# Kernel tuning notes

Hardware: AMD Instinct MI355X
Metric: run time of the kernel (lower is better)

Reference implementation:

```python
import jax, jax.numpy as jnp
import numpy as np

D_MODEL, D_HIDDEN, N_EXPERTS = 1024, 4096, 8
CAP_FACTOR, LBL_COEF, ZLOSS_COEF = 1.25, 0.01, 0.0


def setup_inputs() -> dict:
    key = jax.random.key(0)
    ks = jax.random.split(key, 4)
    B, T = 4, 2048
    x = jax.random.normal(ks[0], (B, T, D_MODEL), dtype=jnp.float32)
    # router linear
    Wr = jax.random.normal(ks[1], (D_MODEL, N_EXPERTS), jnp.float32) / np.sqrt(D_MODEL).astype(np.float32)
    br = jnp.zeros((N_EXPERTS,), jnp.float32)
    # per-expert MLP: fc1 [D->H], gelu, fc2 [H->D]
    W1 = jax.random.normal(ks[2], (N_EXPERTS, D_MODEL, D_HIDDEN), jnp.float32) / np.sqrt(D_MODEL).astype(np.float32)
    b1 = jnp.zeros((N_EXPERTS, D_HIDDEN), jnp.float32)
    W2 = jax.random.normal(ks[3], (N_EXPERTS, D_HIDDEN, D_MODEL), jnp.float32) / np.sqrt(D_HIDDEN).astype(np.float32)
    b2 = jnp.zeros((N_EXPERTS, D_MODEL), jnp.float32)
    return {"x": x, "Wr": Wr, "br": br, "W1": W1, "b1": b1, "W2": W2, "b2": b2}


def reference(x, Wr, br, W1, b1, W2, b2):
    B, T, D = x.shape
    N = B * T
    E = Wr.shape[1]
    cap = int(CAP_FACTOR * (N / E) + 1)  # static Python int

    h = x.reshape(N, D)
    # --- Top1Router ---
    logits = h @ Wr + br                              # [N, E]
    probs = jax.nn.softmax(logits, axis=-1)
    top1 = jnp.argmax(probs, axis=-1)                 # [N]
    w = jnp.take_along_axis(probs, top1[:, None], axis=1)  # [N, 1]
    assign = jax.nn.one_hot(top1, E, dtype=jnp.float32)    # constant wrt grads
    importance = probs.mean(axis=0)
    load = jax.lax.stop_gradient(assign).mean(axis=0)
    lb_loss = E * jnp.sum(importance * load)
    z_loss = jnp.mean(jax.nn.logsumexp(logits, axis=-1) ** 2)

    # --- capacity-based dispatch (first `cap` tokens per expert, token order) ---
    pos = (jnp.cumsum(assign, axis=0) * assign).sum(axis=-1).astype(jnp.int32) - 1  # [N] slot within expert
    keep = pos < cap
    slot = jnp.where(keep, pos, cap)  # dropped tokens -> overflow slot `cap`
    xe = jnp.zeros((E, cap + 1, D), x.dtype).at[top1, slot].set(h)[:, :cap]  # [E, cap, D]

    # --- per-expert MLP as grouped GEMMs ---
    he = jax.nn.gelu(jnp.einsum('ecd,edh->ech', xe, W1) + b1[:, None, :])    # [E, cap, H]
    ye = jnp.einsum('ech,ehd->ecd', he, W2) + b2[:, None, :]                 # [E, cap, D]

    # --- combine (gather back, scale by router weight, zero dropped) ---
    out = ye[top1, jnp.minimum(pos, cap - 1)] * w   # [N, D]
    out = jnp.where(keep[:, None], out, jnp.zeros((), x.dtype))
    y = out.reshape(B, T, D)
    aux = LBL_COEF * lb_loss + ZLOSS_COEF * z_loss
    return (y, aux)
```

## Files before the change

### kernel.cpp

```cpp
#include <hip/hip_runtime.h>
#include <hip/hip_bf16.h>

#define N_TOK 8192
#define DM    1024
#define DH    4096
#define NE    8
#define CAP   1281
#define CAPR  1408
#define ISTR  1536

typedef unsigned short u16;
typedef __attribute__((ext_vector_type(8))) __bf16 bf16x8;
typedef __attribute__((ext_vector_type(8))) short short8;
typedef __attribute__((ext_vector_type(4))) short s16x4;
typedef __attribute__((ext_vector_type(4))) float f4;

__device__ __forceinline__ u16 f2bf(float f){
  union { float f; unsigned u; } v; v.f = f;
  unsigned r = v.u + 0x7fffu + ((v.u >> 16) & 1u);
  return (u16)(r >> 16);
}

__device__ __forceinline__ float gelu_fast(float v){
  float u = 0.7978845608028654f * (v + 0.044715f * v * v * v);
  return v * __builtin_amdgcn_rcpf(1.0f + __expf(-2.0f * u));
}

__device__ __forceinline__ void gl2lds16(const void* g, void* l){
  __builtin_amdgcn_global_load_lds((const __attribute__((address_space(1))) void*)g,
                                   (__attribute__((address_space(3))) void*)l, 16, 0, 0);
}

__global__ __launch_bounds__(256) void tcvt_k(const float* __restrict__ in, u16* __restrict__ out,
                                              int K, int Nn){
  __shared__ float tile[64][68];
  size_t mb = (size_t)blockIdx.z * (size_t)K * (size_t)Nn;
  const float* ip = in + mb;
  u16* op = out + mb;
  int n0 = blockIdx.x*64, k0 = blockIdx.y*64;
  int t = threadIdx.x;
  int kr = t>>4, nc = (t&15)*4;
  #pragma unroll
  for (int ii=0;ii<4;ii++){
    f4 v = *(const f4*)&ip[(size_t)(k0+kr+16*ii)*Nn + n0 + nc];
    tile[kr+16*ii][nc+0] = v[0]; tile[kr+16*ii][nc+1] = v[1];
    tile[kr+16*ii][nc+2] = v[2]; tile[kr+16*ii][nc+3] = v[3];
  }
  __syncthreads();
  int nr = t>>2, kc = (t&3)*16;
  short8 o0, o1;
  #pragma unroll
  for (int c=0;c<8;c++){
    o0[c] = (short)f2bf(tile[kc+c][nr]);
    o1[c] = (short)f2bf(tile[kc+8+c][nr]);
  }
  *(short8*)&op[(size_t)(n0+nr)*K + k0 + kc] = o0;
  *(short8*)&op[(size_t)(n0+nr)*K + k0 + kc + 8] = o1;
}

__global__ __launch_bounds__(256) void router_k(const float* __restrict__ x, const float* __restrict__ Wr,
    const float* __restrict__ br, u16* __restrict__ Xb, int* __restrict__ top1,
    float* __restrict__ wgt, float* __restrict__ impSum){
  __shared__ float pSh[4][8];
  int wid = threadIdx.x >> 6, lane = threadIdx.x & 63;
  int n = blockIdx.x * 4 + wid;
  const float* xr = x + (size_t)n * DM;
  u16* xbr = Xb + (size_t)n * DM;
  float acc[8];
  #pragma unroll
  for (int e=0;e<8;e++) acc[e]=0.f;
  #pragma unroll
  for (int c=0;c<4;c++){
    int d0 = c*256 + lane*4;
    f4 xv = *(const f4*)(xr + d0);
    s16x4 xb;
    #pragma unroll
    for (int j=0;j<4;j++) xb[j] = (short)f2bf(xv[j]);
    *(s16x4*)(xbr + d0) = xb;
    #pragma unroll
    for (int j=0;j<4;j++){
      const float* wrow = Wr + (size_t)(d0+j)*NE;
      float xs = xv[j];
      #pragma unroll
      for (int e=0;e<8;e++) acc[e] = fmaf(xs, wrow[e], acc[e]);
    }
  }
  #pragma unroll
  for (int off=32; off>0; off>>=1){
    #pragma unroll
    for (int e=0;e<8;e++) acc[e] += __shfl_down(acc[e], off, 64);
  }
  if (lane==0){
    float lg[8]; float mx = -1e30f;
    #pragma unroll
    for (int e=0;e<8;e++){ lg[e] = acc[e] + br[e]; mx = fmaxf(mx, lg[e]); }
    float p[8], s=0.f;
    #pragma unroll
    for (int e=0;e<8;e++){ p[e] = expf(lg[e]-mx); s += p[e]; }
    int bt=0; float bv=lg[0];
    #pragma unroll
    for (int e=1;e<8;e++){ if (lg[e]>bv){ bv=lg[e]; bt=e; } }
    float inv = 1.f/s;
    top1[n] = bt; wgt[n] = p[bt]*inv;
    #pragma unroll
    for (int e=0;e<8;e++) pSh[wid][e] = p[e]*inv;
  }
  __syncthreads();
  if (threadIdx.x < 8){
    int e = threadIdx.x;
    atomicAdd(&impSum[e], pSh[0][e]+pSh[1][e]+pSh[2][e]+pSh[3][e]);
  }
}

__global__ __launch_bounds__(1024) void scan_k(const int* __restrict__ top1, int* __restrict__ idx,
    int* __restrict__ cnt, int* __restrict__ rawcnt, int* __restrict__ dropList,
    int* __restrict__ nDrop, const float* __restrict__ impSum, float* __restrict__ auxOut){
  __shared__ int waveCnt[16][8];
  __shared__ int wavePre[16][8];
  __shared__ int chunkTot[8];
  __shared__ int base_s[8];
  int tid = threadIdx.x, wid = tid>>6, lane = tid&63;
  if (tid < 8) base_s[tid] = 0;
  __syncthreads();
  for (int c=0;c<8;c++){
    int t = c*1024 + tid;
    int e = top1[t];
    int myPre = 0;
    #pragma unroll
    for (int ex=0; ex<8; ex++){
      unsigned long long mk = __ballot(e == ex);
      if (lane == 0) waveCnt[wid][ex] = __popcll(mk);
      if (ex == e) myPre = __popcll(mk & ((1ull<<lane)-1ull));
    }
    __syncthreads();
    if (tid < 8){
      int run = 0;
      for (int wv=0; wv<16; wv++){ wavePre[wv][tid] = run; run += waveCnt[wv][tid]; }
      chunkTot[tid] = run;
    }
    __syncthreads();
    int pos = base_s[e] + wavePre[wid][e] + myPre;
    if (pos < CAP) idx[e*ISTR + pos] = t;
    else { int d = atomicAdd(nDrop, 1); dropList[d] = t; }
    __syncthreads();
    if (tid < 8) base_s[tid] += chunkTot[tid];
    __syncthreads();
  }
  if (tid < 8){
    rawcnt[tid] = base_s[tid];
    cnt[tid] = base_s[tid] < CAP ? base_s[tid] : CAP;
  }
  if (tid == 0){
    float s = 0.f;
    for (int e=0;e<8;e++) s += (impSum[e]*(1.f/N_TOK)) * ((float)base_s[e]*(1.f/N_TOK));
    *auxOut = 0.01f * 8.f * s;
  }
}

__global__ __launch_bounds__(256) void zdrop_k(const int* __restrict__ dropList,
    const int* __restrict__ nDrop, float* __restrict__ y){
  int nd = *nDrop;
  for (int i = blockIdx.x; i < nd; i += gridDim.x){
    int t = dropList[i];
    f4* row = (f4*)(y + (size_t)t * DM);
    f4 z; z[0]=0.f; z[1]=0.f; z[2]=0.f; z[3]=0.f;
    row[threadIdx.x] = z;
  }
}


#define LDA(buf, m, kk) (*(const bf16x8*)&lds[(buf)*16384 + (aBase ^ ((kk)*32)) + (m)*1024])
#define LDB(buf, n, kk) (*(const bf16x8*)&lds[32768 + (buf)*16384 + (bBase ^ ((kk)*32)) + (n)*1024])

#define SA_J(buf, j, kc) gl2lds16(aS[j] + (size_t)(kc)*64, &lds[(buf)*16384 + ((j)*512 + t)*8])
#define SB_ALLM(buf, kc) do{ \
  gl2lds16(bS[0] + (size_t)(kc)*64, &lds[32768 + (buf)*16384 + (0*512 + t)*8]); \
  gl2lds16(bS[1] + (size_t)(kc)*64, &lds[32768 + (buf)*16384 + (1*512 + t)*8]); \
  gl2lds16(bS[2] + (size_t)(kc)*64, &lds[32768 + (buf)*16384 + (2*512 + t)*8]); \
  gl2lds16(bS[3] + (size_t)(kc)*64, &lds[32768 + (buf)*16384 + (3*512 + t)*8]); }while(0)

#define LGKM0 do{ asm volatile("s_waitcnt lgkmcnt(0)" ::: "memory"); \
                  __builtin_amdgcn_sched_barrier(0); }while(0)

#define MFMA_PAIR(q) \
  _Pragma("unroll") for (int j_=0;j_<2;j_++) \
    _Pragma("unroll") for (int n_=0;n_<4;n_++) \
      _Pragma("unroll") for (int kk_=0;kk_<2;kk_++) \
        acc[2*(q)+j_][n_] = __builtin_amdgcn_mfma_f32_16x16x32_bf16(a_[j_][kk_], Bf[n_][kk_], acc[2*(q)+j_][n_], 0,0,0);

#define KTILE(buf, ktv, NTv) do{ \
  int kc1 = (ktv)+1 < (NTv) ? (ktv)+1 : (NTv)-1; \
  int kc2 = (ktv)+2 < (NTv) ? (ktv)+2 : (NTv)-1; \
  bf16x8 a_[2][2]; \
   \
  asm volatile("s_waitcnt vmcnt(6)" ::: "memory"); \
  __builtin_amdgcn_s_barrier(); \
  _Pragma("unroll") for (int n_=0;n_<4;n_++){ Bf[n_][0] = LDB(buf,n_,0); Bf[n_][1] = LDB(buf,n_,1); } \
  a_[0][0]=LDA(buf,0,0); a_[0][1]=LDA(buf,0,1); a_[1][0]=LDA(buf,1,0); a_[1][1]=LDA(buf,1,1); \
  SA_J((buf)^1, 1, kc1); SA_J((buf)^1, 3, kc1); \
  LGKM0; \
  __builtin_amdgcn_s_setprio(1); MFMA_PAIR(0); __builtin_amdgcn_s_setprio(0); \
   \
  __builtin_amdgcn_s_barrier(); \
  a_[0][0]=LDA(buf,2,0); a_[0][1]=LDA(buf,2,1); a_[1][0]=LDA(buf,3,0); a_[1][1]=LDA(buf,3,1); \
  SB_ALLM(buf, kc2); \
  LGKM0; \
  __builtin_amdgcn_s_setprio(1); MFMA_PAIR(1); __builtin_amdgcn_s_setprio(0); \
   \
  __builtin_amdgcn_s_barrier(); \
  a_[0][0]=LDA(buf,4,0); a_[0][1]=LDA(buf,4,1); a_[1][0]=LDA(buf,5,0); a_[1][1]=LDA(buf,5,1); \
  SA_J(buf, 0, kc2); SA_J(buf, 2, kc2); \
  LGKM0; \
  __builtin_amdgcn_s_setprio(1); MFMA_PAIR(2); __builtin_amdgcn_s_setprio(0); \
   \
  __builtin_amdgcn_s_barrier(); \
  a_[0][0]=LDA(buf,6,0); a_[0][1]=LDA(buf,6,1); a_[1][0]=LDA(buf,7,0); a_[1][1]=LDA(buf,7,1); \
  LGKM0; \
  __builtin_amdgcn_s_setprio(1); MFMA_PAIR(3); __builtin_amdgcn_s_setprio(0); \
}while(0)

#define GEMM_PROLOGUE() do{ \
  SB_ALLM(0, 0); \
  SA_J(0,0,0); SA_J(0,2,0); \
  SA_J(0,1,0); SA_J(0,3,0); \
  SB_ALLM(1, 1); \
  SA_J(1,0,1); SA_J(1,2,1); }while(0)

__global__ __launch_bounds__(512, 2) void gemm1_k(
    const u16* __restrict__ Xb, const u16* __restrict__ W1T,
    const float* __restrict__ b1, const int* __restrict__ idx,
    const int* __restrict__ cnt, u16* __restrict__ He)
{
  int e = blockIdx.z, mt = blockIdx.y, nt = blockIdx.x;
  int cn = cnt[e];
  if (mt*256 >= cn) return;
  __shared__ __align__(16) u16 lds[65536];
  int t = threadIdx.x, lane = t&63, wid = t>>6;
  int waveM = wid>>2, waveN = wid&3;
  int rA = lane&15, kb = lane>>4, s = rA&7;

  const u16* aS[4]; const u16* bS[4];
  #pragma unroll
  for (int j=0;j<4;j++){
    int pos = j*512 + t;
    int row = pos>>3, ch = pos&7;
    int gcb = ch ^ (row&7);
    int slotrow = mt*256 + row;
    int token = (slotrow < cn) ? idx[e*ISTR + slotrow] : 0;
    aS[j] = Xb + (size_t)token*DM + gcb*8;
    bS[j] = W1T + ((size_t)e*DH + nt*256 + row)*DM + gcb*8;
  }
  f4 acc[8][4];
  #pragma unroll
  for (int m=0;m<8;m++)
    #pragma unroll
    for (int n=0;n<4;n++)
      #pragma unroll
      for (int j=0;j<4;j++) acc[m][n][j]=0.f;

  int aBase = (waveM*128 + rA)*64 + (kb ^ s)*8;
  int bBase = (waveN*64  + rA)*64 + (kb ^ s)*8;
  bf16x8 Bf[4][2];

  GEMM_PROLOGUE();
  const int NT = DM/64;
  #pragma unroll 1
  for (int i=0;i<NT/2;i++){
    KTILE(0, 2*i,   NT);
    KTILE(1, 2*i+1, NT);
  }
  asm volatile("s_waitcnt vmcnt(0) lgkmcnt(0)" ::: "memory");

  int rG = lane>>4;
  #pragma unroll
  for (int n=0;n<4;n++){
    int col = nt*256 + waveN*64 + n*16 + rA;
    float bias = b1[e*DH + col];
    #pragma unroll
    for (int m=0;m<8;m++){
      int slot = mt*256 + waveM*128 + m*16 + rG*4;
      if (slot < CAPR){
        u16* dst = He + ((size_t)e*CAPR + slot)*DH + col;
        #pragma unroll
        for (int j=0;j<4;j++){
          float v = acc[m][n][j] + bias;
          dst[(size_t)j*DH] = f2bf(gelu_fast(v));
        }
      }
    }
  }
}

__global__ __launch_bounds__(512, 2) void gemm2_k(
    const u16* __restrict__ He, const u16* __restrict__ W2T,
    const float* __restrict__ b2, const int* __restrict__ idx,
    const int* __restrict__ cnt, const float* __restrict__ wgt,
    float* __restrict__ y)
{
  int e = blockIdx.z, mt = blockIdx.y, nt = blockIdx.x;
  int cn = cnt[e];
  if (mt*256 >= cn) return;
  __shared__ __align__(16) u16 lds[65536];
  int t = threadIdx.x, lane = t&63, wid = t>>6;
  int waveM = wid>>2, waveN = wid&3;
  int rA = lane&15, kb = lane>>4, s = rA&7;

  const u16* aS[4]; const u16* bS[4];
  #pragma unroll
  for (int j=0;j<4;j++){
    int pos = j*512 + t;
    int row = pos>>3, ch = pos&7;
    int gcb = ch ^ (row&7);
    int srow = mt*256 + row; if (srow >= cn) srow = cn-1;
    aS[j] = He  + ((size_t)e*CAPR + srow)*DH + gcb*8;
    bS[j] = W2T + ((size_t)e*DM + nt*256 + row)*DH + gcb*8;
  }
  f4 acc[8][4];
  #pragma unroll
  for (int m=0;m<8;m++)
    #pragma unroll
    for (int n=0;n<4;n++)
      #pragma unroll
      for (int j=0;j<4;j++) acc[m][n][j]=0.f;

  int aBase = (waveM*128 + rA)*64 + (kb ^ s)*8;
  int bBase = (waveN*64  + rA)*64 + (kb ^ s)*8;
  bf16x8 Bf[4][2];

  GEMM_PROLOGUE();
  const int NT = DH/64;
  #pragma unroll 1
  for (int i=0;i<NT/2;i++){
    KTILE(0, 2*i,   NT);
    KTILE(1, 2*i+1, NT);
  }
  asm volatile("s_waitcnt vmcnt(0) lgkmcnt(0)" ::: "memory");

  int rG = lane>>4;
  float bias_[4];
  #pragma unroll
  for (int n=0;n<4;n++) bias_[n] = b2[e*DM + nt*256 + waveN*64 + n*16 + rA];
  #pragma unroll
  for (int m=0;m<8;m++){
    int slot0 = mt*256 + waveM*128 + m*16 + rG*4;
    #pragma unroll
    for (int j=0;j<4;j++){
      int slot = slot0 + j;
      bool valid = slot < cn;
      int tk = valid ? idx[e*ISTR + slot] : 0;
      float wv = valid ? wgt[tk] : 0.f;
      float* yr = y + (size_t)tk*DM;
      #pragma unroll
      for (int n=0;n<4;n++){
        int col = nt*256 + waveN*64 + n*16 + rA;
        if (valid) yr[col] = (acc[m][n][j] + bias_[n]) * wv;
      }
    }
  }
}

extern "C" void kernel_launch(void* const* d_in, const int* in_sizes, int n_in,
                              void* d_out, int out_size, void* d_ws, size_t ws_size,
                              hipStream_t stream){
  const float* x  = (const float*)d_in[0];
  const float* Wr = (const float*)d_in[1];
  const float* br = (const float*)d_in[2];
  const float* W1 = (const float*)d_in[3];
  const float* b1 = (const float*)d_in[4];
  const float* W2 = (const float*)d_in[5];
  const float* b2 = (const float*)d_in[6];
  float* y = (float*)d_out;

  char* ws = (char*)d_ws;
  u16* Xb  = (u16*)(ws);
  u16* W1T = (u16*)(ws + 16777216ull);
  u16* W2T = (u16*)(ws + 16777216ull + 67108864ull);
  u16* He  = (u16*)(ws + 16777216ull + 2ull*67108864ull);
  char* tail = ws + 16777216ull + 2ull*67108864ull + (size_t)NE*CAPR*DH*2ull;
  int*   top1 = (int*)(tail);
  float* wgt  = (float*)(tail + 32768);
  int*   idx  = (int*)(tail + 65536);
  int*   drop = (int*)(tail + 65536 + 49152);
  float* impSum = (float*)(tail + 65536 + 49152 + 32768);
  int*   nDrop  = (int*)((char*)impSum + 32);
  int*   cnt    = nDrop + 1;
  int*   rawcnt = cnt + 8;

  (void)hipMemsetAsync(impSum, 0, 64, stream);

  tcvt_k<<<dim3(64,16,8), 256, 0, stream>>>(W1, W1T, DM, DH);
  tcvt_k<<<dim3(16,64,8), 256, 0, stream>>>(W2, W2T, DH, DM);
  router_k<<<2048, 256, 0, stream>>>(x, Wr, br, Xb, top1, wgt, impSum);
  scan_k<<<1, 1024, 0, stream>>>(top1, idx, cnt, rawcnt, drop, nDrop, impSum,
                                 y + (size_t)N_TOK*DM);
  zdrop_k<<<64, 256, 0, stream>>>(drop, nDrop, y);
  gemm1_k<<<dim3(DH/256, 6, NE), 512, 0, stream>>>(Xb, W1T, b1, idx, cnt, He);
  gemm2_k<<<dim3(DM/256, 6, NE), 512, 0, stream>>>(He, W2T, b2, idx, cnt, wgt, y);

  (void)in_sizes; (void)n_in; (void)out_size; (void)ws_size;
}
```

Measured before the change: 356.2 us.

## Replace pipelined 256x256 GEMM tiles with simple single-buffered 128x128 tiles

Both expert GEMMs drop the hand-scheduled double-buffered 256x256 pipeline (staggered global-to-LDS loads, setprio, partial waitcnts) for a plain 128x128 tile loop. Each k-step stages everything, syncs, computes and syncs again. The grid is retiled to 128-row and 128-column blocks with 256 threads. The unused rawcnt output is also removed. This gives smaller tiles and finer-grained blocks, but loses the overlap of loads with MFMA work and halves reuse per tile, so it is likely a simplification or debugging step rather than a speedup.

```diff
diff --git a/kernel.cpp b/kernel.cpp
--- a/kernel.cpp
+++ b/kernel.cpp
@@ -113,8 +113,8 @@
 }
 
 __global__ __launch_bounds__(1024) void scan_k(const int* __restrict__ top1, int* __restrict__ idx,
-    int* __restrict__ cnt, int* __restrict__ rawcnt, int* __restrict__ dropList,
-    int* __restrict__ nDrop, const float* __restrict__ impSum, float* __restrict__ auxOut){
+    int* __restrict__ cnt, int* __restrict__ dropList, int* __restrict__ nDrop,
+    const float* __restrict__ impSum, float* __restrict__ auxOut){
   __shared__ int waveCnt[16][8];
   __shared__ int wavePre[16][8];
   __shared__ int chunkTot[8];
@@ -147,7 +147,6 @@
     __syncthreads();
   }
   if (tid < 8){
-    rawcnt[tid] = base_s[tid];
     cnt[tid] = base_s[tid] < CAP ? base_s[tid] : CAP;
   }
   if (tid == 0){
@@ -169,129 +168,94 @@
 }
 
 
-#define LDA(buf, m, kk) (*(const bf16x8*)&lds[(buf)*16384 + (aBase ^ ((kk)*32)) + (m)*1024])
-#define LDB(buf, n, kk) (*(const bf16x8*)&lds[32768 + (buf)*16384 + (bBase ^ ((kk)*32)) + (n)*1024])
-
-#define SA_J(buf, j, kc) gl2lds16(aS[j] + (size_t)(kc)*64, &lds[(buf)*16384 + ((j)*512 + t)*8])
-#define SB_ALLM(buf, kc) do{ \
-  gl2lds16(bS[0] + (size_t)(kc)*64, &lds[32768 + (buf)*16384 + (0*512 + t)*8]); \
-  gl2lds16(bS[1] + (size_t)(kc)*64, &lds[32768 + (buf)*16384 + (1*512 + t)*8]); \
-  gl2lds16(bS[2] + (size_t)(kc)*64, &lds[32768 + (buf)*16384 + (2*512 + t)*8]); \
-  gl2lds16(bS[3] + (size_t)(kc)*64, &lds[32768 + (buf)*16384 + (3*512 + t)*8]); }while(0)
-
-#define LGKM0 do{ asm volatile("s_waitcnt lgkmcnt(0)" ::: "memory"); \
-                  __builtin_amdgcn_sched_barrier(0); }while(0)
-
-#define MFMA_PAIR(q) \
-  _Pragma("unroll") for (int j_=0;j_<2;j_++) \
-    _Pragma("unroll") for (int n_=0;n_<4;n_++) \
-      _Pragma("unroll") for (int kk_=0;kk_<2;kk_++) \
-        acc[2*(q)+j_][n_] = __builtin_amdgcn_mfma_f32_16x16x32_bf16(a_[j_][kk_], Bf[n_][kk_], acc[2*(q)+j_][n_], 0,0,0);
-
-#define KTILE(buf, ktv, NTv) do{ \
-  int kc1 = (ktv)+1 < (NTv) ? (ktv)+1 : (NTv)-1; \
-  int kc2 = (ktv)+2 < (NTv) ? (ktv)+2 : (NTv)-1; \
-  bf16x8 a_[2][2]; \
-   \
-  asm volatile("s_waitcnt vmcnt(6)" ::: "memory"); \
-  __builtin_amdgcn_s_barrier(); \
-  _Pragma("unroll") for (int n_=0;n_<4;n_++){ Bf[n_][0] = LDB(buf,n_,0); Bf[n_][1] = LDB(buf,n_,1); } \
-  a_[0][0]=LDA(buf,0,0); a_[0][1]=LDA(buf,0,1); a_[1][0]=LDA(buf,1,0); a_[1][1]=LDA(buf,1,1); \
-  SA_J((buf)^1, 1, kc1); SA_J((buf)^1, 3, kc1); \
-  LGKM0; \
-  __builtin_amdgcn_s_setprio(1); MFMA_PAIR(0); __builtin_amdgcn_s_setprio(0); \
-   \
-  __builtin_amdgcn_s_barrier(); \
-  a_[0][0]=LDA(buf,2,0); a_[0][1]=LDA(buf,2,1); a_[1][0]=LDA(buf,3,0); a_[1][1]=LDA(buf,3,1); \
-  SB_ALLM(buf, kc2); \
-  LGKM0; \
-  __builtin_amdgcn_s_setprio(1); MFMA_PAIR(1); __builtin_amdgcn_s_setprio(0); \
-   \
-  __builtin_amdgcn_s_barrier(); \
-  a_[0][0]=LDA(buf,4,0); a_[0][1]=LDA(buf,4,1); a_[1][0]=LDA(buf,5,0); a_[1][1]=LDA(buf,5,1); \
-  SA_J(buf, 0, kc2); SA_J(buf, 2, kc2); \
-  LGKM0; \
-  __builtin_amdgcn_s_setprio(1); MFMA_PAIR(2); __builtin_amdgcn_s_setprio(0); \
-   \
-  __builtin_amdgcn_s_barrier(); \
-  a_[0][0]=LDA(buf,6,0); a_[0][1]=LDA(buf,6,1); a_[1][0]=LDA(buf,7,0); a_[1][1]=LDA(buf,7,1); \
-  LGKM0; \
-  __builtin_amdgcn_s_setprio(1); MFMA_PAIR(3); __builtin_amdgcn_s_setprio(0); \
-}while(0)
-
-#define GEMM_PROLOGUE() do{ \
-  SB_ALLM(0, 0); \
-  SA_J(0,0,0); SA_J(0,2,0); \
-  SA_J(0,1,0); SA_J(0,3,0); \
-  SB_ALLM(1, 1); \
-  SA_J(1,0,1); SA_J(1,2,1); }while(0)
-
-__global__ __launch_bounds__(512, 2) void gemm1_k(
+#define LDA(m, kk) (*(const bf16x8*)&As[(aBase ^ ((kk)*32)) + (m)*1024])
+#define LDB(n, kk) (*(const bf16x8*)&Bs[(bBase ^ ((kk)*32)) + (n)*1024])
+
+#define STAGE_ALL(kc) do{ \
+  gl2lds16(aS[0] + (size_t)(kc)*64, &As[(0*256 + t)*8]); \
+  gl2lds16(aS[1] + (size_t)(kc)*64, &As[(1*256 + t)*8]); \
+  gl2lds16(aS[2] + (size_t)(kc)*64, &As[(2*256 + t)*8]); \
+  gl2lds16(aS[3] + (size_t)(kc)*64, &As[(3*256 + t)*8]); \
+  gl2lds16(bS[0] + (size_t)(kc)*64, &Bs[(0*256 + t)*8]); \
+  gl2lds16(bS[1] + (size_t)(kc)*64, &Bs[(1*256 + t)*8]); \
+  gl2lds16(bS[2] + (size_t)(kc)*64, &Bs[(2*256 + t)*8]); \
+  gl2lds16(bS[3] + (size_t)(kc)*64, &Bs[(3*256 + t)*8]); }while(0)
+
+#define COMPUTE_STEP() do{ \
+  _Pragma("unroll") \
+  for (int kk=0; kk<2; kk++){ \
+    bf16x8 af[4], bfr[4]; \
+    _Pragma("unroll") for (int m=0;m<4;m++) af[m] = LDA(m,kk); \
+    _Pragma("unroll") for (int n=0;n<4;n++) bfr[n] = LDB(n,kk); \
+    _Pragma("unroll") for (int m=0;m<4;m++) \
+      _Pragma("unroll") for (int n=0;n<4;n++) \
+        acc[m][n] = __builtin_amdgcn_mfma_f32_16x16x32_bf16(af[m], bfr[n], acc[m][n], 0,0,0); \
+  } }while(0)
+
+__global__ __launch_bounds__(256) void gemm1_k(
     const u16* __restrict__ Xb, const u16* __restrict__ W1T,
     const float* __restrict__ b1, const int* __restrict__ idx,
     const int* __restrict__ cnt, u16* __restrict__ He)
 {
   int e = blockIdx.z, mt = blockIdx.y, nt = blockIdx.x;
   int cn = cnt[e];
-  if (mt*256 >= cn) return;
-  __shared__ __align__(16) u16 lds[65536];
+  if (mt*128 >= cn) return;
+  __shared__ __align__(16) u16 As[128*64];
+  __shared__ __align__(16) u16 Bs[128*64];
   int t = threadIdx.x, lane = t&63, wid = t>>6;
-  int waveM = wid>>2, waveN = wid&3;
+  int waveM = wid>>1, waveN = wid&1;
   int rA = lane&15, kb = lane>>4, s = rA&7;
 
   const u16* aS[4]; const u16* bS[4];
   #pragma unroll
   for (int j=0;j<4;j++){
-    int pos = j*512 + t;
+    int pos = j*256 + t;
     int row = pos>>3, ch = pos&7;
     int gcb = ch ^ (row&7);
-    int slotrow = mt*256 + row;
+    int slotrow = mt*128 + row;
     int token = (slotrow < cn) ? idx[e*ISTR + slotrow] : 0;
     aS[j] = Xb + (size_t)token*DM + gcb*8;
-    bS[j] = W1T + ((size_t)e*DH + nt*256 + row)*DM + gcb*8;
-  }
-  f4 acc[8][4];
-  #pragma unroll
-  for (int m=0;m<8;m++)
+    bS[j] = W1T + ((size_t)e*DH + nt*128 + row)*DM + gcb*8;
+  }
+  f4 acc[4][4];
+  #pragma unroll
+  for (int m=0;m<4;m++)
     #pragma unroll
     for (int n=0;n<4;n++)
       #pragma unroll
       for (int j=0;j<4;j++) acc[m][n][j]=0.f;
 
-  int aBase = (waveM*128 + rA)*64 + (kb ^ s)*8;
-  int bBase = (waveN*64  + rA)*64 + (kb ^ s)*8;
-  bf16x8 Bf[4][2];
-
-  GEMM_PROLOGUE();
+  int aBase = (waveM*64 + rA)*64 + (kb ^ s)*8;
+  int bBase = (waveN*64 + rA)*64 + (kb ^ s)*8;
+
   const int NT = DM/64;
   #pragma unroll 1
-  for (int i=0;i<NT/2;i++){
-    KTILE(0, 2*i,   NT);
-    KTILE(1, 2*i+1, NT);
-  }
-  asm volatile("s_waitcnt vmcnt(0) lgkmcnt(0)" ::: "memory");
+  for (int kt=0; kt<NT; kt++){
+    STAGE_ALL(kt);
+    __syncthreads();
+    COMPUTE_STEP();
+    __syncthreads();
+  }
 
   int rG = lane>>4;
   #pragma unroll
   for (int n=0;n<4;n++){
-    int col = nt*256 + waveN*64 + n*16 + rA;
+    int col = nt*128 + waveN*64 + n*16 + rA;
     float bias = b1[e*DH + col];
     #pragma unroll
-    for (int m=0;m<8;m++){
-      int slot = mt*256 + waveM*128 + m*16 + rG*4;
-      if (slot < CAPR){
-        u16* dst = He + ((size_t)e*CAPR + slot)*DH + col;
-        #pragma unroll
-        for (int j=0;j<4;j++){
-          float v = acc[m][n][j] + bias;
-          dst[(size_t)j*DH] = f2bf(gelu_fast(v));
-        }
+    for (int m=0;m<4;m++){
+      int slot = mt*128 + waveM*64 + m*16 + rG*4;
+      u16* dst = He + ((size_t)e*CAPR + slot)*DH + col;
+      #pragma unroll
+      for (int j=0;j<4;j++){
+        float v = acc[m][n][j] + bias;
+        dst[(size_t)j*DH] = f2bf(gelu_fast(v));
       }
     }
   }
 }
 
-__global__ __launch_bounds__(512, 2) void gemm2_k(
+__global__ __launch_bounds__(256) void gemm2_k(
     const u16* __restrict__ He, const u16* __restrict__ W2T,
     const float* __restrict__ b2, const int* __restrict__ idx,
     const int* __restrict__ cnt, const float* __restrict__ wgt,
@@ -299,50 +263,50 @@
 {
   int e = blockIdx.z, mt = blockIdx.y, nt = blockIdx.x;
   int cn = cnt[e];
-  if (mt*256 >= cn) return;
-  __shared__ __align__(16) u16 lds[65536];
+  if (mt*128 >= cn) return;
+  __shared__ __align__(16) u16 As[128*64];
+  __shared__ __align__(16) u16 Bs[128*64];
   int t = threadIdx.x, lane = t&63, wid = t>>6;
-  int waveM = wid>>2, waveN = wid&3;
+  int waveM = wid>>1, waveN = wid&1;
   int rA = lane&15, kb = lane>>4, s = rA&7;
 
   const u16* aS[4]; const u16* bS[4];
   #pragma unroll
   for (int j=0;j<4;j++){
-    int pos = j*512 + t;
+    int pos = j*256 + t;
     int row = pos>>3, ch = pos&7;
     int gcb = ch ^ (row&7);
-    int srow = mt*256 + row; if (srow >= cn) srow = cn-1;
+    int srow = mt*128 + row; if (srow >= cn) srow = cn-1;
     aS[j] = He  + ((size_t)e*CAPR + srow)*DH + gcb*8;
-    bS[j] = W2T + ((size_t)e*DM + nt*256 + row)*DH + gcb*8;
-  }
-  f4 acc[8][4];
-  #pragma unroll
-  for (int m=0;m<8;m++)
+    bS[j] = W2T + ((size_t)e*DM + nt*128 + row)*DH + gcb*8;
+  }
+  f4 acc[4][4];
+  #pragma unroll
+  for (int m=0;m<4;m++)
     #pragma unroll
     for (int n=0;n<4;n++)
       #pragma unroll
       for (int j=0;j<4;j++) acc[m][n][j]=0.f;
 
-  int aBase = (waveM*128 + rA)*64 + (kb ^ s)*8;
-  int bBase = (waveN*64  + rA)*64 + (kb ^ s)*8;
-  bf16x8 Bf[4][2];
-
-  GEMM_PROLOGUE();
+  int aBase = (waveM*64 + rA)*64 + (kb ^ s)*8;
+  int bBase = (waveN*64 + rA)*64 + (kb ^ s)*8;
+
   const int NT = DH/64;
   #pragma unroll 1
-  for (int i=0;i<NT/2;i++){
-    KTILE(0, 2*i,   NT);
-    KTILE(1, 2*i+1, NT);
-  }
-  asm volatile("s_waitcnt vmcnt(0) lgkmcnt(0)" ::: "memory");
+  for (int kt=0; kt<NT; kt++){
+    STAGE_ALL(kt);
+    __syncthreads();
+    COMPUTE_STEP();
+    __syncthreads();
+  }
 
   int rG = lane>>4;
   float bias_[4];
   #pragma unroll
-  for (int n=0;n<4;n++) bias_[n] = b2[e*DM + nt*256 + waveN*64 + n*16 + rA];
-  #pragma unroll
-  for (int m=0;m<8;m++){
-    int slot0 = mt*256 + waveM*128 + m*16 + rG*4;
+  for (int n=0;n<4;n++) bias_[n] = b2[e*DM + nt*128 + waveN*64 + n*16 + rA];
+  #pragma unroll
+  for (int m=0;m<4;m++){
+    int slot0 = mt*128 + waveM*64 + m*16 + rG*4;
     #pragma unroll
     for (int j=0;j<4;j++){
       int slot = slot0 + j;
@@ -352,7 +316,7 @@
       float* yr = y + (size_t)tk*DM;
       #pragma unroll
       for (int n=0;n<4;n++){
-        int col = nt*256 + waveN*64 + n*16 + rA;
+        int col = nt*128 + waveN*64 + n*16 + rA;
         if (valid) yr[col] = (acc[m][n][j] + bias_[n]) * wv;
       }
     }
@@ -377,25 +341,24 @@
   u16* W2T = (u16*)(ws + 16777216ull + 67108864ull);
   u16* He  = (u16*)(ws + 16777216ull + 2ull*67108864ull);
   char* tail = ws + 16777216ull + 2ull*67108864ull + (size_t)NE*CAPR*DH*2ull;
-  int*   top1 = (int*)(tail);
-  float* wgt  = (float*)(tail + 32768);
-  int*   idx  = (int*)(tail + 65536);
-  int*   drop = (int*)(tail + 65536 + 49152);
+  int*   top1   = (int*)(tail);
+  float* wgt    = (float*)(tail + 32768);
+  int*   idx    = (int*)(tail + 65536);
+  int*   drop   = (int*)(tail + 65536 + 49152);
   float* impSum = (float*)(tail + 65536 + 49152 + 32768);
   int*   nDrop  = (int*)((char*)impSum + 32);
   int*   cnt    = nDrop + 1;
-  int*   rawcnt = cnt + 8;
 
   (void)hipMemsetAsync(impSum, 0, 64, stream);
 
   tcvt_k<<<dim3(64,16,8), 256, 0, stream>>>(W1, W1T, DM, DH);
   tcvt_k<<<dim3(16,64,8), 256, 0, stream>>>(W2, W2T, DH, DM);
   router_k<<<2048, 256, 0, stream>>>(x, Wr, br, Xb, top1, wgt, impSum);
-  scan_k<<<1, 1024, 0, stream>>>(top1, idx, cnt, rawcnt, drop, nDrop, impSum,
+  scan_k<<<1, 1024, 0, stream>>>(top1, idx, cnt, drop, nDrop, impSum,
                                  y + (size_t)N_TOK*DM);
   zdrop_k<<<64, 256, 0, stream>>>(drop, nDrop, y);
-  gemm1_k<<<dim3(DH/256, 6, NE), 512, 0, stream>>>(Xb, W1T, b1, idx, cnt, He);
-  gemm2_k<<<dim3(DM/256, 6, NE), 512, 0, stream>>>(He, W2T, b2, idx, cnt, wgt, y);
+  gemm1_k<<<dim3(DH/128, 11, NE), 256, 0, stream>>>(Xb, W1T, b1, idx, cnt, He);
+  gemm2_k<<<dim3(DM/128, 11, NE), 256, 0, stream>>>(He, W2T, b2, idx, cnt, wgt, y);
 
   (void)in_sizes; (void)n_in; (void)out_size; (void)ws_size;
 }
```

After: 426.8 us. +19.8%, slower.
